# Kernel tuning notes

Hardware: AMD Instinct MI355X
Metric: run time of the kernel (lower is better)

Reference implementation:

```python
import jax, jax.numpy as jnp
import numpy as np

N = 100000   # number of nodes
E = 400000   # number of edges
C = 16       # n_in_channels == n_out_channels
L = 16       # node_conv2 .. node_conv17
EPS = 1e-5   # BatchNorm eps


def _bn(h, g, b):
    # training-mode BatchNorm1d over the edge/batch axis (biased variance)
    mu = h.mean(0)
    var = h.var(0)
    return (h - mu) * jax.lax.rsqrt(var + EPS) * g + b


def setup_inputs() -> dict:
    key = jax.random.key(0)
    ks = jax.random.split(key, 6)
    return {
        "edge_features": jax.random.normal(ks[0], (E, C), jnp.float32),
        "edge_index": jax.random.randint(ks[1], (2, E), 0, N),
        "angles": jax.random.normal(ks[2], (E,), jnp.float32),
        "Wn": jax.random.normal(ks[3], (L, C, 2 * C), jnp.float32) / np.sqrt(2.0 * C),
        "bn": jnp.zeros((L, C), jnp.float32),
        "gn": jnp.ones((L, C), jnp.float32),
        "btn": jnp.zeros((L, C), jnp.float32),
        "We": jax.random.normal(ks[4], (C, 2 * C), jnp.float32) / np.sqrt(2.0 * C),
        "be": jnp.zeros((C,), jnp.float32),
        "ge": jnp.ones((C,), jnp.float32),
        "bte": jnp.zeros((C,), jnp.float32),
    }


def _forward(edge_features, edge_index, Wn, bn, gn, btn, We, be, ge, bte):
    src, dst = edge_index[0], edge_index[1]

    # EdgeConvNoNodes: init node features = mean of incident edge features (both endpoints)
    idx = jnp.concatenate([src, dst])                       # [2E]
    feats = jnp.concatenate([edge_features, edge_features], axis=0)
    deg = jax.ops.segment_sum(jnp.ones((2 * E,), edge_features.dtype), idx, N)
    x = jax.ops.segment_sum(feats, idx, N) / jnp.clip(deg, 1.0)[:, None]  # [N, C]

    # in-degree for mean aggregation of the 16 NodeConv1 layers
    deg_in = jnp.clip(jax.ops.segment_sum(jnp.ones((E,), x.dtype), dst, N), 1.0)[:, None]

    def step(x, p):
        W, b, g, bt = p
        # message: Linear(cat(x_i, x_j)) -> BN -> LeakyReLU on [E, C]
        m = jnp.concatenate([x[dst], x[src]], axis=1) @ W.T + b
        m = jax.nn.leaky_relu(_bn(m, g, bt))
        # mean aggregation at target nodes
        return jax.ops.segment_sum(m, dst, N) / deg_in, None

    x, _ = jax.lax.scan(step, x, (Wn, bn, gn, btn))

    # EdgeConv2: per-edge MLP on both edge directions, BN stats shared over [2E]
    pair = jnp.concatenate(
        [jnp.concatenate([x[src], x[dst]], axis=1),
         jnp.concatenate([x[dst], x[src]], axis=1)], axis=0)  # [2E, 2C]
    e = jax.nn.leaky_relu(_bn(pair @ We.T + be, ge, bte))      # [2E, C]
    e_fwd, e_bwd = e[:E], e[E:]
    edge_out = 0.5 * (e_fwd + e_bwd)                           # symmetric edge feature
    side_loss = jnp.mean((e_fwd - e_bwd) ** 2)                 # symmetry side loss
    return edge_out, side_loss


def reference(edge_features, edge_index, angles, Wn, bn, gn, btn, We, be, ge, bte):
    # `angles` is accepted but unused, matching the original forward
    return _forward(edge_features, edge_index, Wn, bn, gn, btn, We, be, ge, bte)
```

## Files before the change

### kernel.cpp

```cpp
#include <hip/hip_runtime.h>
#include <hip/hip_fp16.h>
#include <cstdint>
#include <cstddef>

#define NN 100000
#define EE 400000
#define CC 16
#define LL 16
#define NB 8

typedef unsigned int uint;

__device__ __forceinline__ float lrelu(float v){ return v > 0.0f ? v : 0.01f*v; }

__device__ __forceinline__ float waveSum(float v){
#pragma unroll
  for (int off = 32; off >= 1; off >>= 1) v += __shfl_xor(v, off);
  return v;
}

__device__ __forceinline__ float fma4(float4 w, float4 v, float a){
  a = fmaf(w.x, v.x, a); a = fmaf(w.y, v.y, a);
  a = fmaf(w.z, v.z, a); a = fmaf(w.w, v.w, a);
  return a;
}

__device__ __forceinline__ uint pack_h2(float a, float b){
  __half2 h = __floats2half2_rn(a, b);
  return *reinterpret_cast<uint*>(&h);
}
__device__ __forceinline__ float2 unpack_h2(uint v){
  __half2 h = *reinterpret_cast<__half2*>(&v);
  return __half22float2(h);
}

__global__ __launch_bounds__(256) void k_count(const int* __restrict__ ei,
    int* __restrict__ cdst, int* __restrict__ call)
{
  int t = blockIdx.x*256 + threadIdx.x;
  if (t >= EE) return;
  int s = ei[t], d = ei[EE + t];
  atomicAdd(&cdst[d], 1);
  atomicAdd(&call[s], 1);
  atomicAdd(&call[d], 1);
}

__device__ __forceinline__ void scan_one(const int* __restrict__ cnt,
    int* __restrict__ rp, int* __restrict__ bsums, int n, int* sd)
{
  int tid = threadIdx.x;
  int base = blockIdx.x*1024 + tid*4;
  int v0=0,v1=0,v2=0,v3=0;
  if (base+0 < n) v0 = cnt[base+0];
  if (base+1 < n) v1 = cnt[base+1];
  if (base+2 < n) v2 = cnt[base+2];
  if (base+3 < n) v3 = cnt[base+3];
  int tot = v0+v1+v2+v3;
  sd[tid] = tot; __syncthreads();
  for (int off=1; off<256; off<<=1){
    int add = (tid>=off) ? sd[tid-off] : 0;
    __syncthreads();
    sd[tid] += add;
    __syncthreads();
  }
  int excl = sd[tid] - tot;
  if (base+0 < n) rp[base+0] = excl;
  if (base+1 < n) rp[base+1] = excl+v0;
  if (base+2 < n) rp[base+2] = excl+v0+v1;
  if (base+3 < n) rp[base+3] = excl+v0+v1+v2;
  if (tid==255) bsums[blockIdx.x] = sd[255];
  __syncthreads();
}

__global__ __launch_bounds__(256) void k_scan1(const int* __restrict__ ca,
    int* __restrict__ rpa, int* __restrict__ bsa,
    const int* __restrict__ cb, int* __restrict__ rpb, int* __restrict__ bsb, int n)
{
  __shared__ int sd[256];
  scan_one(ca, rpa, bsa, n, sd);
  scan_one(cb, rpb, bsb, n, sd);
}

__device__ __forceinline__ void scan2_one(const int* __restrict__ bsums,
    int* __restrict__ boff, int nseg, int* sd)
{
  int tid = threadIdx.x;
  int v = (tid < nseg) ? bsums[tid] : 0;
  sd[tid] = v; __syncthreads();
  for (int off=1; off<256; off<<=1){
    int add = (tid>=off) ? sd[tid-off] : 0;
    __syncthreads();
    sd[tid] += add;
    __syncthreads();
  }
  if (tid < nseg) boff[tid] = sd[tid] - v;
  __syncthreads();
}

__global__ __launch_bounds__(256) void k_scan2(const int* __restrict__ bsa,
    int* __restrict__ boffa, const int* __restrict__ bsb, int* __restrict__ boffb, int nseg)
{
  __shared__ int sd[256];
  scan2_one(bsa, boffa, nseg, sd);
  scan2_one(bsb, boffb, nseg, sd);
}

__global__ __launch_bounds__(256) void k_scan3(
    int* __restrict__ rpa, int* __restrict__ cura, const int* __restrict__ boffa, int totala,
    int* __restrict__ rpb, int* __restrict__ curb, const int* __restrict__ boffb, int totalb, int n)
{
  int adda = boffa[blockIdx.x];
  int addb = boffb[blockIdx.x];
  int base = blockIdx.x*1024 + threadIdx.x*4;
#pragma unroll
  for (int i=0;i<4;i++){
    if (base+i < n){
      int va = rpa[base+i] + adda; rpa[base+i] = va; cura[base+i] = va;
      int vb = rpb[base+i] + addb; rpb[base+i] = vb; curb[base+i] = vb;
    }
  }
  if (blockIdx.x==0 && threadIdx.x==0){ rpa[n] = totala; rpb[n] = totalb; }
}

__global__ __launch_bounds__(256) void k_fill(const int* __restrict__ ei,
    int* __restrict__ cur, int2* __restrict__ sd,
    int* __restrict__ cur_all, int* __restrict__ list_all)
{
  int t = blockIdx.x*256 + threadIdx.x;
  if (t >= EE) return;
  int s = ei[t], d = ei[EE + t];
  int p = atomicAdd(&cur[d], 1);
  sd[p] = make_int2(s, d);
  int pa = atomicAdd(&cur_all[s], 1);
  list_all[pa] = t;
  int pb = atomicAdd(&cur_all[d], 1);
  list_all[pb] = t;
}

__global__ __launch_bounds__(256) void k_gather0(const float* __restrict__ ef,
    const int* __restrict__ rp_all, const int* __restrict__ list_all,
    const int* __restrict__ rp, float* __restrict__ x0, float* __restrict__ invdeg)
{
  int t = blockIdx.x*256 + threadIdx.x;
  if (t >= NN*CC) return;
  int n = t >> 4, c = t & 15;
  int beg = rp_all[n], end = rp_all[n+1];
  float acc = 0.0f;
  for (int i=beg; i<end; i++){
    acc += ef[(size_t)list_all[i]*CC + c];
  }
  float dg = fmaxf((float)(end-beg), 1.0f);
  x0[t] = acc / dg;
  if (c == 0){
    int di = rp[n+1] - rp[n];
    invdeg[n] = 1.0f / fmaxf((float)di, 1.0f);
  }
}

__global__ __launch_bounds__(256) void k_edge(const float* __restrict__ x,
    const int2* __restrict__ sd,
    const float* __restrict__ W, const float* __restrict__ b,
    uint* __restrict__ mh, double* __restrict__ st)
{
  __shared__ float sW[512];
  __shared__ float sb16[16];
  __shared__ float sredS[64], sredQ[64];
  for (int i=threadIdx.x; i<512; i+=256) sW[i] = W[i];
  if (threadIdx.x < 16) sb16[threadIdx.x] = b[threadIdx.x];
  __syncthreads();

  int t = blockIdx.x*256 + threadIdx.x;
  int e0 = 2*t, e1 = 2*t+1;
  bool val = (e1 < EE);
  float acc0[16], acc1[16];
  if (val){
    int2 p0 = sd[e0], p1 = sd[e1];
    float4 xc0[8], xc1[8];
    const float4* p;
    p = (const float4*)(x + (size_t)p0.y*CC); xc0[0]=p[0]; xc0[1]=p[1]; xc0[2]=p[2]; xc0[3]=p[3];
    p = (const float4*)(x + (size_t)p0.x*CC); xc0[4]=p[0]; xc0[5]=p[1]; xc0[6]=p[2]; xc0[7]=p[3];
    p = (const float4*)(x + (size_t)p1.y*CC); xc1[0]=p[0]; xc1[1]=p[1]; xc1[2]=p[2]; xc1[3]=p[3];
    p = (const float4*)(x + (size_t)p1.x*CC); xc1[4]=p[0]; xc1[5]=p[1]; xc1[6]=p[2]; xc1[7]=p[3];
#pragma unroll
    for (int c=0;c<CC;c++){
      const float4* wr = (const float4*)(sW + c*32);
      float a0 = sb16[c], a1 = sb16[c];
#pragma unroll
      for (int q=0;q<8;q++){
        float4 w = wr[q];
        a0 = fma4(w, xc0[q], a0);
        a1 = fma4(w, xc1[q], a1);
      }
      acc0[c]=a0; acc1[c]=a1;
    }
    uint w0[8], w1[8];
#pragma unroll
    for (int q=0;q<8;q++){
      w0[q] = pack_h2(acc0[2*q], acc0[2*q+1]);
      w1[q] = pack_h2(acc1[2*q], acc1[2*q+1]);
    }
    uint4* po0 = (uint4*)(mh + (size_t)e0*8);
    po0[0] = make_uint4(w0[0],w0[1],w0[2],w0[3]);
    po0[1] = make_uint4(w0[4],w0[5],w0[6],w0[7]);
    uint4* po1 = (uint4*)(mh + (size_t)e1*8);
    po1[0] = make_uint4(w1[0],w1[1],w1[2],w1[3]);
    po1[1] = make_uint4(w1[4],w1[5],w1[6],w1[7]);
  } else {
#pragma unroll
    for (int c=0;c<CC;c++){ acc0[c]=0.0f; acc1[c]=0.0f; }
  }

  int lane = threadIdx.x & 63, w = threadIdx.x >> 6;
#pragma unroll
  for (int c=0;c<CC;c++){
    float rs = acc0[c] + acc1[c];
    float rq = acc0[c]*acc0[c] + acc1[c]*acc1[c];
    rs = waveSum(rs); rq = waveSum(rq);
    if (lane == 0){ sredS[w*16+c] = rs; sredQ[w*16+c] = rq; }
  }
  __syncthreads();
  double* stb = st + (size_t)(blockIdx.x & (NB-1))*32;
  if (threadIdx.x < 16){
    int c = threadIdx.x;
    float tot = sredS[c] + sredS[16+c] + sredS[32+c] + sredS[48+c];
    unsafeAtomicAdd(&stb[c], (double)tot);
  } else if (threadIdx.x < 32){
    int c = threadIdx.x - 16;
    float tot = sredQ[c] + sredQ[16+c] + sredQ[32+c] + sredQ[48+c];
    unsafeAtomicAdd(&stb[16+c], (double)tot);
  }
}

__global__ __launch_bounds__(256) void k_node(const uint* __restrict__ mh,
    const int* __restrict__ rp,
    const float* __restrict__ invdeg, const double* __restrict__ st,
    const float* __restrict__ g, const float* __restrict__ bt,
    float* __restrict__ xout)
{
  __shared__ float sA[16], sB[16];
  if (threadIdx.x < 16){
    int c = threadIdx.x;
    double S = 0.0, Q = 0.0;
#pragma unroll
    for (int k=0;k<NB;k++){ S += st[k*32 + c]; Q += st[k*32 + 16 + c]; }
    double mu  = S * (1.0/EE);
    double var = Q * (1.0/EE) - mu*mu;
    float sc = rsqrtf((float)var + 1e-5f);
    float A = sc * g[c];
    sA[c] = A; sB[c] = bt[c] - (float)mu * A;
  }
  __syncthreads();
  int t = blockIdx.x*256 + threadIdx.x;
  int n = t >> 3, cp = t & 7;
  if (n >= NN) return;
  float A0 = sA[2*cp], B0 = sB[2*cp];
  float A1 = sA[2*cp+1], B1 = sB[2*cp+1];
  int beg = rp[n], end = rp[n+1];
  float a0 = 0.0f, a1 = 0.0f;
  for (int i=beg; i<end; i++){
    float2 v = unpack_h2(mh[(size_t)i*8 + cp]);
    a0 += lrelu(fmaf(A0, v.x, B0));
    a1 += lrelu(fmaf(A1, v.y, B1));
  }
  float iv = invdeg[n];
  float2* po = (float2*)(xout + (size_t)n*CC + 2*cp);
  *po = make_float2(a0*iv, a1*iv);
}

__global__ __launch_bounds__(256) void k_final1(const float* __restrict__ x,
    const int* __restrict__ ei, const float* __restrict__ W, const float* __restrict__ b,
    double* __restrict__ st)
{
  __shared__ float sW[512];
  __shared__ float sb16[16];
  __shared__ float sredS[64], sredQ[64];
  for (int i=threadIdx.x; i<512; i+=256) sW[i] = W[i];
  if (threadIdx.x < 16) sb16[threadIdx.x] = b[threadIdx.x];
  __syncthreads();

  int t = blockIdx.x*256 + threadIdx.x;
  bool val = (t < EE);
  float af[16], ab[16];
  if (val){
    int s = ei[t], d = ei[EE+t];
    float4 xs[4], xd[4];
    const float4* p;
    p = (const float4*)(x + (size_t)s*CC); xs[0]=p[0]; xs[1]=p[1]; xs[2]=p[2]; xs[3]=p[3];
    p = (const float4*)(x + (size_t)d*CC); xd[0]=p[0]; xd[1]=p[1]; xd[2]=p[2]; xd[3]=p[3];
#pragma unroll
    for (int c=0;c<CC;c++){
      const float4* wr = (const float4*)(sW + c*32);
      float f = sb16[c], g_ = sb16[c];
#pragma unroll
      for (int q=0;q<4;q++){ float4 w = wr[q];   f = fma4(w, xs[q], f);  g_ = fma4(w, xd[q], g_); }
#pragma unroll
      for (int q=0;q<4;q++){ float4 w = wr[4+q]; f = fma4(w, xd[q], f);  g_ = fma4(w, xs[q], g_); }
      af[c]=f; ab[c]=g_;
    }
  } else {
#pragma unroll
    for (int c=0;c<CC;c++){ af[c]=0.0f; ab[c]=0.0f; }
  }

  int lane = threadIdx.x & 63, w = threadIdx.x >> 6;
#pragma unroll
  for (int c=0;c<CC;c++){
    float rs = af[c] + ab[c];
    float rq = af[c]*af[c] + ab[c]*ab[c];
    rs = waveSum(rs); rq = waveSum(rq);
    if (lane == 0){ sredS[w*16+c] = rs; sredQ[w*16+c] = rq; }
  }
  __syncthreads();
  double* stb = st + (size_t)(blockIdx.x & (NB-1))*32;
  if (threadIdx.x < 16){
    int c = threadIdx.x;
    float tot = sredS[c] + sredS[16+c] + sredS[32+c] + sredS[48+c];
    unsafeAtomicAdd(&stb[c], (double)tot);
  } else if (threadIdx.x < 32){
    int c = threadIdx.x - 16;
    float tot = sredQ[c] + sredQ[16+c] + sredQ[32+c] + sredQ[48+c];
    unsafeAtomicAdd(&stb[16+c], (double)tot);
  }
}

__global__ __launch_bounds__(256) void k_final2(const float* __restrict__ x,
    const int* __restrict__ ei, const float* __restrict__ W, const float* __restrict__ b,
    const double* __restrict__ st, const float* __restrict__ g, const float* __restrict__ bt,
    float* __restrict__ out, double* __restrict__ loss)
{
  __shared__ float sW[512];
  __shared__ float sb16[16];
  __shared__ float sA[16], sB[16];
  __shared__ float sl[4];
  for (int i=threadIdx.x; i<512; i+=256) sW[i] = W[i];
  if (threadIdx.x < 16){
    int c = threadIdx.x;
    sb16[c] = b[c];
    double S = 0.0, Q = 0.0;
#pragma unroll
    for (int k=0;k<NB;k++){ S += st[k*32 + c]; Q += st[k*32 + 16 + c]; }
    double mu  = S * (1.0/(2.0*EE));
    double var = Q * (1.0/(2.0*EE)) - mu*mu;
    float sc = rsqrtf((float)var + 1e-5f);
    float A = sc * g[c];
    sA[c] = A; sB[c] = bt[c] - (float)mu * A;
  }
  __syncthreads();

  int t = blockIdx.x*256 + threadIdx.x;
  bool val = (t < EE);
  float lsum = 0.0f;
  if (val){
    int s = ei[t], d = ei[EE+t];
    float4 xs[4], xd[4];
    const float4* p;
    p = (const float4*)(x + (size_t)s*CC); xs[0]=p[0]; xs[1]=p[1]; xs[2]=p[2]; xs[3]=p[3];
    p = (const float4*)(x + (size_t)d*CC); xd[0]=p[0]; xd[1]=p[1]; xd[2]=p[2]; xd[3]=p[3];
    float fo[16];
#pragma unroll
    for (int c=0;c<CC;c++){
      const float4* wr = (const float4*)(sW + c*32);
      float f = sb16[c], g_ = sb16[c];
#pragma unroll
      for (int q=0;q<4;q++){ float4 w = wr[q];   f = fma4(w, xs[q], f);  g_ = fma4(w, xd[q], g_); }
#pragma unroll
      for (int q=0;q<4;q++){ float4 w = wr[4+q]; f = fma4(w, xd[q], f);  g_ = fma4(w, xs[q], g_); }
      float efv = lrelu(fmaf(sA[c], f,  sB[c]));
      float ebv = lrelu(fmaf(sA[c], g_, sB[c]));
      fo[c] = 0.5f*(efv + ebv);
      float dlt = efv - ebv;
      lsum = fmaf(dlt, dlt, lsum);
    }
    float4* po = (float4*)(out + (size_t)t*CC);
    po[0]=make_float4(fo[0],fo[1],fo[2],fo[3]);
    po[1]=make_float4(fo[4],fo[5],fo[6],fo[7]);
    po[2]=make_float4(fo[8],fo[9],fo[10],fo[11]);
    po[3]=make_float4(fo[12],fo[13],fo[14],fo[15]);
  }
  lsum = waveSum(lsum);
  int lane = threadIdx.x & 63, w = threadIdx.x >> 6;
  if (lane == 0) sl[w] = lsum;
  __syncthreads();
  if (threadIdx.x == 0)
    unsafeAtomicAdd(&loss[blockIdx.x & (NB-1)], (double)(sl[0]+sl[1]+sl[2]+sl[3]));
}

__global__ void k_final3(float* __restrict__ out, const double* __restrict__ loss)
{
  double s = 0.0;
#pragma unroll
  for (int k=0;k<NB;k++) s += loss[k];
  out[(size_t)EE*CC] = (float)(s * (1.0/((double)EE*CC)));
}

extern "C" void kernel_launch(void* const* d_in, const int* in_sizes, int n_in,
                              void* d_out, int out_size, void* d_ws, size_t ws_size,
                              hipStream_t stream)
{
  (void)in_sizes; (void)n_in; (void)out_size; (void)ws_size;
  const float* ef  = (const float*)d_in[0];
  const int*   ei  = (const int*)d_in[1];
  const float* Wn  = (const float*)d_in[3];
  const float* bn  = (const float*)d_in[4];
  const float* gn  = (const float*)d_in[5];
  const float* btn = (const float*)d_in[6];
  const float* We  = (const float*)d_in[7];
  const float* be  = (const float*)d_in[8];
  const float* ge  = (const float*)d_in[9];
  const float* bte = (const float*)d_in[10];
  float* out = (float*)d_out;
  char* ws = (char*)d_ws;

  size_t off = 0;
  auto alloc = [&](size_t bytes)->size_t{
    size_t r = off; off = (off + bytes + 255) & ~(size_t)255; return r;
  };
  size_t o_xa     = alloc((size_t)NN*CC*4);
  size_t o_xb     = alloc((size_t)NN*CC*4);
  size_t o_mh     = alloc((size_t)EE*8*4);
  size_t o_cdst   = alloc((size_t)NN*4);
  size_t o_call   = alloc((size_t)NN*4);
  size_t o_rp     = alloc((size_t)(NN+1)*4);
  size_t o_rpall  = alloc((size_t)(NN+1)*4);
  size_t o_cur    = alloc((size_t)NN*4);
  size_t o_curall = alloc((size_t)NN*4);
  size_t o_sd     = alloc((size_t)EE*8);
  size_t o_listall= alloc((size_t)2*EE*4);
  size_t o_bsum   = alloc(512);
  size_t o_bsum2  = alloc(512);
  size_t o_boff   = alloc(512);
  size_t o_boff2  = alloc(512);
  size_t o_stats  = alloc((size_t)(17*NB*32 + NB)*8);
  size_t o_invdeg = alloc((size_t)NN*4);

  float*  x_a     = (float*)(ws + o_xa);
  float*  x_b     = (float*)(ws + o_xb);
  uint*   m_h     = (uint*)(ws + o_mh);
  int*    cdst    = (int*)(ws + o_cdst);
  int*    call_   = (int*)(ws + o_call);
  int*    rp      = (int*)(ws + o_rp);
  int*    rp_all  = (int*)(ws + o_rpall);
  int*    cur     = (int*)(ws + o_cur);
  int*    cur_all = (int*)(ws + o_curall);
  int2*   sd      = (int2*)(ws + o_sd);
  int*    list_all= (int*)(ws + o_listall);
  int*    bsum    = (int*)(ws + o_bsum);
  int*    bsum2   = (int*)(ws + o_bsum2);
  int*    boff    = (int*)(ws + o_boff);
  int*    boff2   = (int*)(ws + o_boff2);
  double* stats   = (double*)(ws + o_stats);
  double* lossd   = stats + (size_t)17*NB*32;
  float*  invdeg  = (float*)(ws + o_invdeg);

  const int GB_E  = (EE + 255)/256;
  const int GB_E2 = (EE/2 + 255)/256;
  const int GB_NC = (NN*CC + 255)/256;
  const int GB_N8 = (NN*8 + 255)/256;
  const int NSEG  = (NN + 1023)/1024;

  hipMemsetAsync(cdst, 0, (size_t)NN*4, stream);
  hipMemsetAsync(call_, 0, (size_t)NN*4, stream);
  hipMemsetAsync(stats, 0, (size_t)(17*NB*32 + NB)*8, stream);

  k_count<<<GB_E, 256, 0, stream>>>(ei, cdst, call_);
  k_scan1<<<NSEG, 256, 0, stream>>>(cdst, rp, bsum, call_, rp_all, bsum2, NN);
  k_scan2<<<1, 256, 0, stream>>>(bsum, boff, bsum2, boff2, NSEG);
  k_scan3<<<NSEG, 256, 0, stream>>>(rp, cur, boff, EE, rp_all, cur_all, boff2, 2*EE, NN);
  k_fill<<<GB_E, 256, 0, stream>>>(ei, cur, sd, cur_all, list_all);
  k_gather0<<<GB_NC, 256, 0, stream>>>(ef, rp_all, list_all, rp, x_a, invdeg);

  const float* xc = x_a;
  float* xn = x_b;
  for (int l = 0; l < LL; ++l){
    double* st = stats + (size_t)l*NB*32;
    const float* Wl = Wn + (size_t)l*CC*2*CC;
    const float* bl = bn + (size_t)l*CC;
    k_edge<<<GB_E2, 256, 0, stream>>>(xc, sd, Wl, bl, m_h, st);
    k_node<<<GB_N8, 256, 0, stream>>>(m_h, rp, invdeg, st,
                                      gn + (size_t)l*CC, btn + (size_t)l*CC, xn);
    float* tmp = (float*)xc; xc = xn; xn = tmp;
  }

  double* stF = stats + (size_t)16*NB*32;
  k_final1<<<GB_E, 256, 0, stream>>>(xc, ei, We, be, stF);
  k_final2<<<GB_E, 256, 0, stream>>>(xc, ei, We, be, stF, ge, bte, out, lossd);
  k_final3<<<1, 1, 0, stream>>>(out, lossd);
}
```

Before: 865.4 us.

## Fuse all layers and final edge MLP into one cooperative persistent kernel

Replaces the 34 per-layer edge/node/final kernel launches with a single cooperative kernel that loops over layers, using grid.sync between the BN-statistics and aggregation phases. Each block owns a contiguous node range and its incoming edges, so messages are kept in LDS (up to 1024 edges per block) rather than going through global memory, spilling to global only on overflow. It adds grid-wide barriers and limits parallelism to one resident grid (at most 1024 blocks), and falls back to the old multi-kernel path if the cooperative launch fails.

```diff
diff --git a/kernel.cpp b/kernel.cpp
--- a/kernel.cpp
+++ b/kernel.cpp
@@ -1,5 +1,6 @@
 #include <hip/hip_runtime.h>
 #include <hip/hip_fp16.h>
+#include <hip/hip_cooperative_groups.h>
 #include <cstdint>
 #include <cstddef>
 
@@ -8,7 +9,10 @@
 #define CC 16
 #define LL 16
 #define NB 8
-
+#define CAP 1024
+#define CSTR 1032
+
+namespace cg = cooperative_groups;
 typedef unsigned int uint;
 
 __device__ __forceinline__ float lrelu(float v){ return v > 0.0f ? v : 0.01f*v; }
@@ -157,7 +161,246 @@
   }
 }
 
-__global__ __launch_bounds__(256) void k_edge(const float* __restrict__ x,
+__global__ __launch_bounds__(256) void k_layers(
+    float* __restrict__ xa, float* __restrict__ xb,
+    const int2* __restrict__ sd, const int* __restrict__ rp,
+    const float* __restrict__ invdeg, const int* __restrict__ ei,
+    const float* __restrict__ Wn, const float* __restrict__ bn,
+    const float* __restrict__ gn, const float* __restrict__ btn,
+    const float* __restrict__ We, const float* __restrict__ be,
+    const float* __restrict__ ge, const float* __restrict__ bte,
+    double* __restrict__ stats, double* __restrict__ lossd,
+    uint* __restrict__ mspill, float* __restrict__ out)
+{
+  cg::grid_group grid = cg::this_grid();
+  __shared__ float sW[512];
+  __shared__ float sb[16];
+  __shared__ float sAB[32];
+  __shared__ float sredS[64], sredQ[64];
+  __shared__ float sl[4];
+  __shared__ uint  sM[8*CSTR];
+
+  const int tid = threadIdx.x;
+  const int bid = blockIdx.x;
+  const int nblk = gridDim.x;
+  const int npb = (NN + nblk - 1) / nblk;
+  int nlo = bid * npb; if (nlo > NN) nlo = NN;
+  int nhi = nlo + npb; if (nhi > NN) nhi = NN;
+  const int ebeg = rp[nlo];
+  const int eend = rp[nhi];
+
+  const float* xc = xa;
+  float* xn = xb;
+
+  float ls[16], lq[16];
+
+  for (int l = 0; l < LL; ++l){
+    const float* W = Wn + (size_t)l*512;
+    for (int i = tid; i < 512; i += 256) sW[i] = W[i];
+    if (tid < 16) sb[tid] = bn[l*16 + tid];
+    __syncthreads();
+
+#pragma unroll
+    for (int c=0;c<16;c++){ ls[c]=0.f; lq[c]=0.f; }
+
+    for (int i = ebeg + tid; i < eend; i += 256){
+      int2 p = sd[i];
+      const float4* xd4 = (const float4*)(xc + (size_t)p.y*CC);
+      const float4* xs4 = (const float4*)(xc + (size_t)p.x*CC);
+      float4 xd0=xd4[0], xd1=xd4[1], xd2=xd4[2], xd3=xd4[3];
+      float4 xs0=xs4[0], xs1=xs4[1], xs2=xs4[2], xs3=xs4[3];
+      int slot = i - ebeg;
+      bool inl = slot < CAP;
+      uint* gsp = mspill + (size_t)i*8;
+#pragma unroll
+      for (int q = 0; q < 8; ++q){
+        const int c = 2*q;
+        const float4* w0 = (const float4*)(sW + c*32);
+        const float4* w1 = (const float4*)(sW + c*32 + 32);
+        float a0 = sb[c], a1 = sb[c+1];
+        a0 = fma4(w0[0],xd0,a0); a0 = fma4(w0[1],xd1,a0);
+        a0 = fma4(w0[2],xd2,a0); a0 = fma4(w0[3],xd3,a0);
+        a0 = fma4(w0[4],xs0,a0); a0 = fma4(w0[5],xs1,a0);
+        a0 = fma4(w0[6],xs2,a0); a0 = fma4(w0[7],xs3,a0);
+        a1 = fma4(w1[0],xd0,a1); a1 = fma4(w1[1],xd1,a1);
+        a1 = fma4(w1[2],xd2,a1); a1 = fma4(w1[3],xd3,a1);
+        a1 = fma4(w1[4],xs0,a1); a1 = fma4(w1[5],xs1,a1);
+        a1 = fma4(w1[6],xs2,a1); a1 = fma4(w1[7],xs3,a1);
+        ls[c]   += a0; lq[c]   += a0*a0;
+        ls[c+1] += a1; lq[c+1] += a1*a1;
+        uint pk = pack_h2(a0, a1);
+        if (inl) sM[q*CSTR + slot] = pk; else gsp[q] = pk;
+      }
+    }
+
+    {
+      int lane = tid & 63, w = tid >> 6;
+#pragma unroll
+      for (int c=0;c<16;c++){
+        float rs = waveSum(ls[c]);
+        float rq = waveSum(lq[c]);
+        if (lane==0){ sredS[w*16+c]=rs; sredQ[w*16+c]=rq; }
+      }
+      __syncthreads();
+      double* stb = stats + (size_t)l*NB*32 + (size_t)(bid & (NB-1))*32;
+      if (tid < 16){
+        float tot = sredS[tid]+sredS[16+tid]+sredS[32+tid]+sredS[48+tid];
+        unsafeAtomicAdd(&stb[tid], (double)tot);
+      } else if (tid < 32){
+        int c = tid-16;
+        float tot = sredQ[c]+sredQ[16+c]+sredQ[32+c]+sredQ[48+c];
+        unsafeAtomicAdd(&stb[16+c], (double)tot);
+      }
+    }
+    __threadfence();
+    grid.sync();
+
+    if (tid < 16){
+      const double* stl = stats + (size_t)l*NB*32;
+      double S=0.0, Q=0.0;
+#pragma unroll
+      for (int k=0;k<NB;k++){ S += stl[k*32+tid]; Q += stl[k*32+16+tid]; }
+      double mu  = S * (1.0/EE);
+      double var = Q * (1.0/EE) - mu*mu;
+      float sc = rsqrtf((float)var + 1e-5f);
+      float A = sc * gn[l*16+tid];
+      sAB[tid] = A; sAB[16+tid] = btn[l*16+tid] - (float)mu * A;
+    }
+    __syncthreads();
+
+    for (int u = tid; u < npb*8; u += 256){
+      int n = nlo + (u>>3);
+      if (n >= nhi) break;
+      int cp = u & 7;
+      float A0=sAB[2*cp],   B0=sAB[16+2*cp];
+      float A1=sAB[2*cp+1], B1=sAB[16+2*cp+1];
+      int beg = rp[n], end = rp[n+1];
+      float a0=0.f, a1=0.f;
+      for (int i=beg; i<end; ++i){
+        int slot = i - ebeg;
+        uint v = (slot < CAP) ? sM[cp*CSTR + slot] : mspill[(size_t)i*8 + cp];
+        float2 f = unpack_h2(v);
+        a0 += lrelu(fmaf(A0, f.x, B0));
+        a1 += lrelu(fmaf(A1, f.y, B1));
+      }
+      float iv = invdeg[n];
+      *(float2*)(xn + (size_t)n*CC + 2*cp) = make_float2(a0*iv, a1*iv);
+    }
+    __threadfence();
+    grid.sync();
+    const float* t = xc; xc = xn; xn = (float*)t;
+  }
+
+  for (int i = tid; i < 512; i += 256) sW[i] = We[i];
+  if (tid < 16) sb[tid] = be[tid];
+  __syncthreads();
+
+  const int epb = (EE + nblk - 1) / nblk;
+  int fb = bid*epb; if (fb > EE) fb = EE;
+  int fe = fb + epb; if (fe > EE) fe = EE;
+
+#pragma unroll
+  for (int c=0;c<16;c++){ ls[c]=0.f; lq[c]=0.f; }
+  for (int t_ = fb + tid; t_ < fe; t_ += 256){
+    int s = ei[t_], d = ei[EE+t_];
+    const float4* ps = (const float4*)(xc + (size_t)s*CC);
+    const float4* pd = (const float4*)(xc + (size_t)d*CC);
+    float4 xs0=ps[0], xs1=ps[1], xs2=ps[2], xs3=ps[3];
+    float4 xd0=pd[0], xd1=pd[1], xd2=pd[2], xd3=pd[3];
+#pragma unroll
+    for (int c=0;c<16;c++){
+      const float4* wr = (const float4*)(sW + c*32);
+      float f = sb[c], g_ = sb[c];
+      f  = fma4(wr[0],xs0,f);  f  = fma4(wr[1],xs1,f);
+      f  = fma4(wr[2],xs2,f);  f  = fma4(wr[3],xs3,f);
+      f  = fma4(wr[4],xd0,f);  f  = fma4(wr[5],xd1,f);
+      f  = fma4(wr[6],xd2,f);  f  = fma4(wr[7],xd3,f);
+      g_ = fma4(wr[0],xd0,g_); g_ = fma4(wr[1],xd1,g_);
+      g_ = fma4(wr[2],xd2,g_); g_ = fma4(wr[3],xd3,g_);
+      g_ = fma4(wr[4],xs0,g_); g_ = fma4(wr[5],xs1,g_);
+      g_ = fma4(wr[6],xs2,g_); g_ = fma4(wr[7],xs3,g_);
+      ls[c] += f + g_;
+      lq[c] += f*f + g_*g_;
+    }
+  }
+  {
+    int lane = tid & 63, w = tid >> 6;
+#pragma unroll
+    for (int c=0;c<16;c++){
+      float rs = waveSum(ls[c]);
+      float rq = waveSum(lq[c]);
+      if (lane==0){ sredS[w*16+c]=rs; sredQ[w*16+c]=rq; }
+    }
+    __syncthreads();
+    double* stb = stats + (size_t)LL*NB*32 + (size_t)(bid & (NB-1))*32;
+    if (tid < 16){
+      float tot = sredS[tid]+sredS[16+tid]+sredS[32+tid]+sredS[48+tid];
+      unsafeAtomicAdd(&stb[tid], (double)tot);
+    } else if (tid < 32){
+      int c = tid-16;
+      float tot = sredQ[c]+sredQ[16+c]+sredQ[32+c]+sredQ[48+c];
+      unsafeAtomicAdd(&stb[16+c], (double)tot);
+    }
+  }
+  __threadfence();
+  grid.sync();
+
+  if (tid < 16){
+    const double* stl = stats + (size_t)LL*NB*32;
+    double S=0.0, Q=0.0;
+#pragma unroll
+    for (int k=0;k<NB;k++){ S += stl[k*32+tid]; Q += stl[k*32+16+tid]; }
+    double mu  = S * (1.0/(2.0*EE));
+    double var = Q * (1.0/(2.0*EE)) - mu*mu;
+    float sc = rsqrtf((float)var + 1e-5f);
+    float A = sc * ge[tid];
+    sAB[tid] = A; sAB[16+tid] = bte[tid] - (float)mu * A;
+  }
+  __syncthreads();
+
+  float lsum = 0.0f;
+  for (int t_ = fb + tid; t_ < fe; t_ += 256){
+    int s = ei[t_], d = ei[EE+t_];
+    const float4* ps = (const float4*)(xc + (size_t)s*CC);
+    const float4* pd = (const float4*)(xc + (size_t)d*CC);
+    float4 xs0=ps[0], xs1=ps[1], xs2=ps[2], xs3=ps[3];
+    float4 xd0=pd[0], xd1=pd[1], xd2=pd[2], xd3=pd[3];
+    float fo[16];
+#pragma unroll
+    for (int c=0;c<16;c++){
+      const float4* wr = (const float4*)(sW + c*32);
+      float f = sb[c], g_ = sb[c];
+      f  = fma4(wr[0],xs0,f);  f  = fma4(wr[1],xs1,f);
+      f  = fma4(wr[2],xs2,f);  f  = fma4(wr[3],xs3,f);
+      f  = fma4(wr[4],xd0,f);  f  = fma4(wr[5],xd1,f);
+      f  = fma4(wr[6],xd2,f);  f  = fma4(wr[7],xd3,f);
+      g_ = fma4(wr[0],xd0,g_); g_ = fma4(wr[1],xd1,g_);
+      g_ = fma4(wr[2],xd2,g_); g_ = fma4(wr[3],xd3,g_);
+      g_ = fma4(wr[4],xs0,g_); g_ = fma4(wr[5],xs1,g_);
+      g_ = fma4(wr[6],xs2,g_); g_ = fma4(wr[7],xs3,g_);
+      float efv = lrelu(fmaf(sAB[c], f,  sAB[16+c]));
+      float ebv = lrelu(fmaf(sAB[c], g_, sAB[16+c]));
+      fo[c] = 0.5f*(efv + ebv);
+      float dlt = efv - ebv;
+      lsum = fmaf(dlt, dlt, lsum);
+    }
+    float4* po = (float4*)(out + (size_t)t_*CC);
+    po[0]=make_float4(fo[0],fo[1],fo[2],fo[3]);
+    po[1]=make_float4(fo[4],fo[5],fo[6],fo[7]);
+    po[2]=make_float4(fo[8],fo[9],fo[10],fo[11]);
+    po[3]=make_float4(fo[12],fo[13],fo[14],fo[15]);
+  }
+  lsum = waveSum(lsum);
+  {
+    int lane = tid & 63, w = tid >> 6;
+    if (lane == 0) sl[w] = lsum;
+    __syncthreads();
+    if (tid == 0)
+      unsafeAtomicAdd(&lossd[bid & (NB-1)], (double)(sl[0]+sl[1]+sl[2]+sl[3]));
+  }
+}
+
+__global__ __launch_bounds__(256) void k_edge_fb(const float* __restrict__ x,
     const int2* __restrict__ sd,
     const float* __restrict__ W, const float* __restrict__ b,
     uint* __restrict__ mh, double* __restrict__ st)
@@ -231,7 +474,7 @@
   }
 }
 
-__global__ __launch_bounds__(256) void k_node(const uint* __restrict__ mh,
+__global__ __launch_bounds__(256) void k_node_fb(const uint* __restrict__ mh,
     const int* __restrict__ rp,
     const float* __restrict__ invdeg, const double* __restrict__ st,
     const float* __restrict__ g, const float* __restrict__ bt,
@@ -267,7 +510,7 @@
   *po = make_float2(a0*iv, a1*iv);
 }
 
-__global__ __launch_bounds__(256) void k_final1(const float* __restrict__ x,
+__global__ __launch_bounds__(256) void k_final1_fb(const float* __restrict__ x,
     const int* __restrict__ ei, const float* __restrict__ W, const float* __restrict__ b,
     double* __restrict__ st)
 {
@@ -323,7 +566,7 @@
   }
 }
 
-__global__ __launch_bounds__(256) void k_final2(const float* __restrict__ x,
+__global__ __launch_bounds__(256) void k_final2_fb(const float* __restrict__ x,
     const int* __restrict__ ei, const float* __restrict__ W, const float* __restrict__ b,
     const double* __restrict__ st, const float* __restrict__ g, const float* __restrict__ bt,
     float* __restrict__ out, double* __restrict__ loss)
@@ -469,20 +712,40 @@
   k_fill<<<GB_E, 256, 0, stream>>>(ei, cur, sd, cur_all, list_all);
   k_gather0<<<GB_NC, 256, 0, stream>>>(ef, rp_all, list_all, rp, x_a, invdeg);
 
-  const float* xc = x_a;
-  float* xn = x_b;
-  for (int l = 0; l < LL; ++l){
-    double* st = stats + (size_t)l*NB*32;
-    const float* Wl = Wn + (size_t)l*CC*2*CC;
-    const float* bl = bn + (size_t)l*CC;
-    k_edge<<<GB_E2, 256, 0, stream>>>(xc, sd, Wl, bl, m_h, st);
-    k_node<<<GB_N8, 256, 0, stream>>>(m_h, rp, invdeg, st,
-                                      gn + (size_t)l*CC, btn + (size_t)l*CC, xn);
-    float* tmp = (float*)xc; xc = xn; xn = tmp;
-  }
-
-  double* stF = stats + (size_t)16*NB*32;
-  k_final1<<<GB_E, 256, 0, stream>>>(xc, ei, We, be, stF);
-  k_final2<<<GB_E, 256, 0, stream>>>(xc, ei, We, be, stF, ge, bte, out, lossd);
+  int occ = 0, cus = 0, dev = 0;
+  (void)hipGetDevice(&dev);
+  (void)hipDeviceGetAttribute(&cus, hipDeviceAttributeMultiprocessorCount, dev);
+  (void)hipOccupancyMaxActiveBlocksPerMultiprocessor(&occ, (const void*)k_layers, 256, 0);
+  long maxg = (long)occ * (long)(cus > 0 ? cus : 0);
+  int grid = (int)(maxg > 1024 ? 1024 : maxg);
+
+  hipError_t cerr = hipErrorUnknown;
+  if (grid >= 64){
+    void* args[] = {
+      (void*)&x_a, (void*)&x_b, (void*)&sd, (void*)&rp, (void*)&invdeg, (void*)&ei,
+      (void*)&Wn, (void*)&bn, (void*)&gn, (void*)&btn,
+      (void*)&We, (void*)&be, (void*)&ge, (void*)&bte,
+      (void*)&stats, (void*)&lossd, (void*)&m_h, (void*)&out
+    };
+    cerr = hipLaunchCooperativeKernel((void*)k_layers, dim3(grid), dim3(256), args, 0, stream);
+  }
+
+  if (cerr != hipSuccess){
+    const float* xc = x_a;
+    float* xn = x_b;
+    for (int l = 0; l < LL; ++l){
+      double* st = stats + (size_t)l*NB*32;
+      const float* Wl = Wn + (size_t)l*CC*2*CC;
+      const float* bl = bn + (size_t)l*CC;
+      k_edge_fb<<<GB_E2, 256, 0, stream>>>(xc, sd, Wl, bl, m_h, st);
+      k_node_fb<<<GB_N8, 256, 0, stream>>>(m_h, rp, invdeg, st,
+                                           gn + (size_t)l*CC, btn + (size_t)l*CC, xn);
+      float* tmp = (float*)xc; xc = xn; xn = tmp;
+    }
+    double* stF = stats + (size_t)LL*NB*32;
+    k_final1_fb<<<GB_E, 256, 0, stream>>>(xc, ei, We, be, stF);
+    k_final2_fb<<<GB_E, 256, 0, stream>>>(xc, ei, We, be, stF, ge, bte, out, lossd);
+  }
+
   k_final3<<<1, 1, 0, stream>>>(out, lossd);
 }
```

Result: no change. 867.5 us (+0.2%).

## Split edge linear into per-node U/V projections and fuse next-layer projection into aggregation

Applied to the files above, without the earlier changes.

Because W·cat(x_dst, x_src) = W1·x_dst + W2·x_src, the per-edge 16x32 matvec becomes two per-node projections (u, v), stored in fp16 and summed per edge. The per-edge message buffer disappears. A stats kernel gathers u[dst] and v[src] to accumulate the BatchNorm sums, and the node kernel recomputes each message from u and v during aggregation. The node kernel also computes the next layer's u and v from the new x through shared memory, so the per-layer matmul cost drops from E to N rows. In exchange every edge is gathered twice per layer, and the pre-BN message is now rounded from the sum of two fp16 values.

```diff
diff --git a/kernel.cpp b/kernel.cpp
--- a/kernel.cpp
+++ b/kernel.cpp
@@ -157,65 +157,77 @@
   }
 }
 
-__global__ __launch_bounds__(256) void k_edge(const float* __restrict__ x,
-    const int2* __restrict__ sd,
+__global__ __launch_bounds__(256) void k_uv(const float* __restrict__ x,
     const float* __restrict__ W, const float* __restrict__ b,
-    uint* __restrict__ mh, double* __restrict__ st)
+    uint* __restrict__ u, uint* __restrict__ v)
 {
   __shared__ float sW[512];
   __shared__ float sb16[16];
-  __shared__ float sredS[64], sredQ[64];
   for (int i=threadIdx.x; i<512; i+=256) sW[i] = W[i];
   if (threadIdx.x < 16) sb16[threadIdx.x] = b[threadIdx.x];
   __syncthreads();
-
+  int n = blockIdx.x*256 + threadIdx.x;
+  if (n >= NN) return;
+  const float4* xr = (const float4*)(x + (size_t)n*CC);
+  float4 x0 = xr[0], x1 = xr[1], x2 = xr[2], x3 = xr[3];
+  uint up[8], vp[8];
+#pragma unroll
+  for (int q=0;q<8;q++){
+    int c0 = 2*q, c1 = 2*q+1;
+    const float4* w0 = (const float4*)(sW + c0*32);
+    const float4* w1 = (const float4*)(sW + c1*32);
+    float u0 = sb16[c0], u1 = sb16[c1], v0 = 0.f, v1 = 0.f;
+    u0 = fma4(w0[0],x0,u0); u0 = fma4(w0[1],x1,u0); u0 = fma4(w0[2],x2,u0); u0 = fma4(w0[3],x3,u0);
+    v0 = fma4(w0[4],x0,v0); v0 = fma4(w0[5],x1,v0); v0 = fma4(w0[6],x2,v0); v0 = fma4(w0[7],x3,v0);
+    u1 = fma4(w1[0],x0,u1); u1 = fma4(w1[1],x1,u1); u1 = fma4(w1[2],x2,u1); u1 = fma4(w1[3],x3,u1);
+    v1 = fma4(w1[4],x0,v1); v1 = fma4(w1[5],x1,v1); v1 = fma4(w1[6],x2,v1); v1 = fma4(w1[7],x3,v1);
+    up[q] = pack_h2(u0,u1);
+    vp[q] = pack_h2(v0,v1);
+  }
+  uint4* pu = (uint4*)(u + (size_t)n*8);
+  pu[0] = make_uint4(up[0],up[1],up[2],up[3]);
+  pu[1] = make_uint4(up[4],up[5],up[6],up[7]);
+  uint4* pv = (uint4*)(v + (size_t)n*8);
+  pv[0] = make_uint4(vp[0],vp[1],vp[2],vp[3]);
+  pv[1] = make_uint4(vp[4],vp[5],vp[6],vp[7]);
+}
+
+__global__ __launch_bounds__(256) void k_stat(
+    const uint* __restrict__ u, const uint* __restrict__ v,
+    const int2* __restrict__ sd, double* __restrict__ st)
+{
+  __shared__ float sredS[64], sredQ[64];
   int t = blockIdx.x*256 + threadIdx.x;
-  int e0 = 2*t, e1 = 2*t+1;
-  bool val = (e1 < EE);
-  float acc0[16], acc1[16];
-  if (val){
-    int2 p0 = sd[e0], p1 = sd[e1];
-    float4 xc0[8], xc1[8];
-    const float4* p;
-    p = (const float4*)(x + (size_t)p0.y*CC); xc0[0]=p[0]; xc0[1]=p[1]; xc0[2]=p[2]; xc0[3]=p[3];
-    p = (const float4*)(x + (size_t)p0.x*CC); xc0[4]=p[0]; xc0[5]=p[1]; xc0[6]=p[2]; xc0[7]=p[3];
-    p = (const float4*)(x + (size_t)p1.y*CC); xc1[0]=p[0]; xc1[1]=p[1]; xc1[2]=p[2]; xc1[3]=p[3];
-    p = (const float4*)(x + (size_t)p1.x*CC); xc1[4]=p[0]; xc1[5]=p[1]; xc1[6]=p[2]; xc1[7]=p[3];
-#pragma unroll
-    for (int c=0;c<CC;c++){
-      const float4* wr = (const float4*)(sW + c*32);
-      float a0 = sb16[c], a1 = sb16[c];
+  float ls[16], lq[16];
+#pragma unroll
+  for (int c=0;c<16;c++){ ls[c]=0.f; lq[c]=0.f; }
+#pragma unroll
+  for (int k=0;k<2;k++){
+    int e = 2*t + k;
+    if (e < EE){
+      int2 p = sd[e];
+      const uint4* pu = (const uint4*)(u + (size_t)p.y*8);
+      const uint4* pv = (const uint4*)(v + (size_t)p.x*8);
+      uint4 ua = pu[0], ub = pu[1];
+      uint4 va = pv[0], vb = pv[1];
+      uint uw[8] = {ua.x,ua.y,ua.z,ua.w, ub.x,ub.y,ub.z,ub.w};
+      uint vw[8] = {va.x,va.y,va.z,va.w, vb.x,vb.y,vb.z,vb.w};
 #pragma unroll
       for (int q=0;q<8;q++){
-        float4 w = wr[q];
-        a0 = fma4(w, xc0[q], a0);
-        a1 = fma4(w, xc1[q], a1);
+        float2 fu = unpack_h2(uw[q]);
+        float2 fv = unpack_h2(vw[q]);
+        float m0 = fu.x + fv.x;
+        float m1 = fu.y + fv.y;
+        ls[2*q]   += m0; lq[2*q]   += m0*m0;
+        ls[2*q+1] += m1; lq[2*q+1] += m1*m1;
       }
-      acc0[c]=a0; acc1[c]=a1;
     }
-    uint w0[8], w1[8];
-#pragma unroll
-    for (int q=0;q<8;q++){
-      w0[q] = pack_h2(acc0[2*q], acc0[2*q+1]);
-      w1[q] = pack_h2(acc1[2*q], acc1[2*q+1]);
-    }
-    uint4* po0 = (uint4*)(mh + (size_t)e0*8);
-    po0[0] = make_uint4(w0[0],w0[1],w0[2],w0[3]);
-    po0[1] = make_uint4(w0[4],w0[5],w0[6],w0[7]);
-    uint4* po1 = (uint4*)(mh + (size_t)e1*8);
-    po1[0] = make_uint4(w1[0],w1[1],w1[2],w1[3]);
-    po1[1] = make_uint4(w1[4],w1[5],w1[6],w1[7]);
-  } else {
-#pragma unroll
-    for (int c=0;c<CC;c++){ acc0[c]=0.0f; acc1[c]=0.0f; }
-  }
-
+  }
   int lane = threadIdx.x & 63, w = threadIdx.x >> 6;
 #pragma unroll
-  for (int c=0;c<CC;c++){
-    float rs = acc0[c] + acc1[c];
-    float rq = acc0[c]*acc0[c] + acc1[c]*acc1[c];
-    rs = waveSum(rs); rq = waveSum(rq);
+  for (int c=0;c<16;c++){
+    float rs = waveSum(ls[c]);
+    float rq = waveSum(lq[c]);
     if (lane == 0){ sredS[w*16+c] = rs; sredQ[w*16+c] = rq; }
   }
   __syncthreads();
@@ -231,15 +243,26 @@
   }
 }
 
-__global__ __launch_bounds__(256) void k_node(const uint* __restrict__ mh,
-    const int* __restrict__ rp,
+template<bool LAST>
+__global__ __launch_bounds__(256) void k_node_uv(
+    const uint* __restrict__ u, const uint* __restrict__ v,
+    const int2* __restrict__ sd, const int* __restrict__ rp,
     const float* __restrict__ invdeg, const double* __restrict__ st,
     const float* __restrict__ g, const float* __restrict__ bt,
-    float* __restrict__ xout)
+    const float* __restrict__ Wnx, const float* __restrict__ bnx,
+    uint* __restrict__ unx, uint* __restrict__ vnx, float* __restrict__ xout)
 {
   __shared__ float sA[16], sB[16];
-  if (threadIdx.x < 16){
-    int c = threadIdx.x;
+  __shared__ float sW[512];
+  __shared__ float sbn[16];
+  __shared__ float sX[32][17];
+  const int tid = threadIdx.x;
+  if (!LAST){
+    for (int i=tid;i<512;i+=256) sW[i] = Wnx[i];
+    if (tid < 16) sbn[tid] = bnx[tid];
+  }
+  if (tid < 16){
+    int c = tid;
     double S = 0.0, Q = 0.0;
 #pragma unroll
     for (int k=0;k<NB;k++){ S += st[k*32 + c]; Q += st[k*32 + 16 + c]; }
@@ -250,21 +273,44 @@
     sA[c] = A; sB[c] = bt[c] - (float)mu * A;
   }
   __syncthreads();
-  int t = blockIdx.x*256 + threadIdx.x;
-  int n = t >> 3, cp = t & 7;
-  if (n >= NN) return;
-  float A0 = sA[2*cp], B0 = sB[2*cp];
+
+  int t = blockIdx.x*256 + tid;
+  int n = t >> 3, cp = t & 7, nl = tid >> 3;
+  float A0 = sA[2*cp],   B0 = sB[2*cp];
   float A1 = sA[2*cp+1], B1 = sB[2*cp+1];
+  float2 uu = unpack_h2(u[(size_t)n*8 + cp]);
   int beg = rp[n], end = rp[n+1];
-  float a0 = 0.0f, a1 = 0.0f;
-  for (int i=beg; i<end; i++){
-    float2 v = unpack_h2(mh[(size_t)i*8 + cp]);
-    a0 += lrelu(fmaf(A0, v.x, B0));
-    a1 += lrelu(fmaf(A1, v.y, B1));
+  float a0 = 0.f, a1 = 0.f;
+  for (int i=beg; i<end; ++i){
+    int s = sd[i].x;
+    float2 fv = unpack_h2(v[(size_t)s*8 + cp]);
+    a0 += lrelu(fmaf(A0, uu.x + fv.x, B0));
+    a1 += lrelu(fmaf(A1, uu.y + fv.y, B1));
   }
   float iv = invdeg[n];
-  float2* po = (float2*)(xout + (size_t)n*CC + 2*cp);
-  *po = make_float2(a0*iv, a1*iv);
+  float xv0 = a0*iv, xv1 = a1*iv;
+
+  if (LAST){
+    *(float2*)(xout + (size_t)n*CC + 2*cp) = make_float2(xv0, xv1);
+  } else {
+    sX[nl][2*cp] = xv0; sX[nl][2*cp+1] = xv1;
+    __syncthreads();
+    int c0 = 2*cp, c1 = 2*cp+1;
+    const float* w0 = sW + c0*32;
+    const float* w1 = sW + c1*32;
+    const float* xr = sX[nl];
+    float un0 = sbn[c0], un1 = sbn[c1], vn0 = 0.f, vn1 = 0.f;
+#pragma unroll
+    for (int k=0;k<16;k++){
+      float xv = xr[k];
+      un0 = fmaf(w0[k],    xv, un0);
+      vn0 = fmaf(w0[16+k], xv, vn0);
+      un1 = fmaf(w1[k],    xv, un1);
+      vn1 = fmaf(w1[16+k], xv, vn1);
+    }
+    unx[(size_t)n*8 + cp] = pack_h2(un0, un1);
+    vnx[(size_t)n*8 + cp] = pack_h2(vn0, vn1);
+  }
 }
 
 __global__ __launch_bounds__(256) void k_final1(const float* __restrict__ x,
@@ -416,8 +462,10 @@
     size_t r = off; off = (off + bytes + 255) & ~(size_t)255; return r;
   };
   size_t o_xa     = alloc((size_t)NN*CC*4);
-  size_t o_xb     = alloc((size_t)NN*CC*4);
-  size_t o_mh     = alloc((size_t)EE*8*4);
+  size_t o_ua     = alloc((size_t)NN*8*4);
+  size_t o_va     = alloc((size_t)NN*8*4);
+  size_t o_ub     = alloc((size_t)NN*8*4);
+  size_t o_vb     = alloc((size_t)NN*8*4);
   size_t o_cdst   = alloc((size_t)NN*4);
   size_t o_call   = alloc((size_t)NN*4);
   size_t o_rp     = alloc((size_t)(NN+1)*4);
@@ -434,8 +482,10 @@
   size_t o_invdeg = alloc((size_t)NN*4);
 
   float*  x_a     = (float*)(ws + o_xa);
-  float*  x_b     = (float*)(ws + o_xb);
-  uint*   m_h     = (uint*)(ws + o_mh);
+  uint*   u_a     = (uint*)(ws + o_ua);
+  uint*   v_a     = (uint*)(ws + o_va);
+  uint*   u_b     = (uint*)(ws + o_ub);
+  uint*   v_b     = (uint*)(ws + o_vb);
   int*    cdst    = (int*)(ws + o_cdst);
   int*    call_   = (int*)(ws + o_call);
   int*    rp      = (int*)(ws + o_rp);
@@ -455,7 +505,8 @@
   const int GB_E  = (EE + 255)/256;
   const int GB_E2 = (EE/2 + 255)/256;
   const int GB_NC = (NN*CC + 255)/256;
-  const int GB_N8 = (NN*8 + 255)/256;
+  const int GB_N8 = (NN*8)/256;
+  const int GB_N  = (NN + 255)/256;
   const int NSEG  = (NN + 1023)/1024;
 
   hipMemsetAsync(cdst, 0, (size_t)NN*4, stream);
@@ -468,21 +519,29 @@
   k_scan3<<<NSEG, 256, 0, stream>>>(rp, cur, boff, EE, rp_all, cur_all, boff2, 2*EE, NN);
   k_fill<<<GB_E, 256, 0, stream>>>(ei, cur, sd, cur_all, list_all);
   k_gather0<<<GB_NC, 256, 0, stream>>>(ef, rp_all, list_all, rp, x_a, invdeg);
-
-  const float* xc = x_a;
-  float* xn = x_b;
+  k_uv<<<GB_N, 256, 0, stream>>>(x_a, Wn, bn, u_a, v_a);
+
+  uint* uc = u_a; uint* vc = v_a;
+  uint* un = u_b; uint* vn = v_b;
   for (int l = 0; l < LL; ++l){
     double* st = stats + (size_t)l*NB*32;
-    const float* Wl = Wn + (size_t)l*CC*2*CC;
-    const float* bl = bn + (size_t)l*CC;
-    k_edge<<<GB_E2, 256, 0, stream>>>(xc, sd, Wl, bl, m_h, st);
-    k_node<<<GB_N8, 256, 0, stream>>>(m_h, rp, invdeg, st,
-                                      gn + (size_t)l*CC, btn + (size_t)l*CC, xn);
-    float* tmp = (float*)xc; xc = xn; xn = tmp;
-  }
-
-  double* stF = stats + (size_t)16*NB*32;
-  k_final1<<<GB_E, 256, 0, stream>>>(xc, ei, We, be, stF);
-  k_final2<<<GB_E, 256, 0, stream>>>(xc, ei, We, be, stF, ge, bte, out, lossd);
+    k_stat<<<GB_E2, 256, 0, stream>>>(uc, vc, sd, st);
+    if (l < LL-1){
+      k_node_uv<false><<<GB_N8, 256, 0, stream>>>(uc, vc, sd, rp, invdeg, st,
+          gn + (size_t)l*CC, btn + (size_t)l*CC,
+          Wn + (size_t)(l+1)*CC*2*CC, bn + (size_t)(l+1)*CC,
+          un, vn, nullptr);
+      uint* t1 = uc; uc = un; un = t1;
+      uint* t2 = vc; vc = vn; vn = t2;
+    } else {
+      k_node_uv<true><<<GB_N8, 256, 0, stream>>>(uc, vc, sd, rp, invdeg, st,
+          gn + (size_t)l*CC, btn + (size_t)l*CC,
+          nullptr, nullptr, nullptr, nullptr, x_a);
+    }
+  }
+
+  double* stF = stats + (size_t)LL*NB*32;
+  k_final1<<<GB_E, 256, 0, stream>>>(x_a, ei, We, be, stF);
+  k_final2<<<GB_E, 256, 0, stream>>>(x_a, ei, We, be, stF, ge, bte, out, lossd);
   k_final3<<<1, 1, 0, stream>>>(out, lossd);
 }
```

Result: slower. 960.8 us (+11.0%).

## Partition edge kernel by destination-node blocks and widen stats atomic spread

Applied to the files above, without the earlier changes.

The per-layer edge kernel now assigns each block a range of 32 destination nodes and loops over their CSR edge range, one edge per thread with strided iteration, instead of two edges per thread over a flat grid. Both edge and node kernels launch NN/32 blocks, and the BN statistics atomics are spread across 32 slots instead of 8 to reduce contention. The goal is fewer double-atomic collisions and more uniform per-thread work. The cost is load imbalance from varying per-block edge counts. The node kernel's bounds check is dropped because the grid now divides NN exactly.

```diff
diff --git a/kernel.cpp b/kernel.cpp
--- a/kernel.cpp
+++ b/kernel.cpp
@@ -7,7 +7,8 @@
 #define EE 400000
 #define CC 16
 #define LL 16
-#define NB 8
+#define NB 32
+#define NPB 32
 
 typedef unsigned int uint;
 
@@ -158,7 +159,7 @@
 }
 
 __global__ __launch_bounds__(256) void k_edge(const float* __restrict__ x,
-    const int2* __restrict__ sd,
+    const int2* __restrict__ sd, const int* __restrict__ rp,
     const float* __restrict__ W, const float* __restrict__ b,
     uint* __restrict__ mh, double* __restrict__ st)
 {
@@ -169,53 +170,48 @@
   if (threadIdx.x < 16) sb16[threadIdx.x] = b[threadIdx.x];
   __syncthreads();
 
-  int t = blockIdx.x*256 + threadIdx.x;
-  int e0 = 2*t, e1 = 2*t+1;
-  bool val = (e1 < EE);
-  float acc0[16], acc1[16];
-  if (val){
-    int2 p0 = sd[e0], p1 = sd[e1];
-    float4 xc0[8], xc1[8];
-    const float4* p;
-    p = (const float4*)(x + (size_t)p0.y*CC); xc0[0]=p[0]; xc0[1]=p[1]; xc0[2]=p[2]; xc0[3]=p[3];
-    p = (const float4*)(x + (size_t)p0.x*CC); xc0[4]=p[0]; xc0[5]=p[1]; xc0[6]=p[2]; xc0[7]=p[3];
-    p = (const float4*)(x + (size_t)p1.y*CC); xc1[0]=p[0]; xc1[1]=p[1]; xc1[2]=p[2]; xc1[3]=p[3];
-    p = (const float4*)(x + (size_t)p1.x*CC); xc1[4]=p[0]; xc1[5]=p[1]; xc1[6]=p[2]; xc1[7]=p[3];
-#pragma unroll
-    for (int c=0;c<CC;c++){
-      const float4* wr = (const float4*)(sW + c*32);
-      float a0 = sb16[c], a1 = sb16[c];
-#pragma unroll
-      for (int q=0;q<8;q++){
-        float4 w = wr[q];
-        a0 = fma4(w, xc0[q], a0);
-        a1 = fma4(w, xc1[q], a1);
-      }
-      acc0[c]=a0; acc1[c]=a1;
+  int nlo = blockIdx.x * NPB;
+  int elo = rp[nlo], ehi = rp[nlo + NPB];
+
+  float ls[16], lq[16];
+#pragma unroll
+  for (int c=0;c<16;c++){ ls[c]=0.f; lq[c]=0.f; }
+
+  for (int i = elo + threadIdx.x; i < ehi; i += 256){
+    int2 p = sd[i];
+    const float4* xd4 = (const float4*)(x + (size_t)p.y*CC);
+    const float4* xs4 = (const float4*)(x + (size_t)p.x*CC);
+    float4 xd0=xd4[0], xd1=xd4[1], xd2=xd4[2], xd3=xd4[3];
+    float4 xs0=xs4[0], xs1=xs4[1], xs2=xs4[2], xs3=xs4[3];
+    uint pk[8];
+#pragma unroll
+    for (int q=0;q<8;q++){
+      int c0 = 2*q, c1 = 2*q+1;
+      const float4* w0 = (const float4*)(sW + c0*32);
+      const float4* w1 = (const float4*)(sW + c1*32);
+      float a0 = sb16[c0], a1 = sb16[c1];
+      a0 = fma4(w0[0],xd0,a0); a0 = fma4(w0[1],xd1,a0);
+      a0 = fma4(w0[2],xd2,a0); a0 = fma4(w0[3],xd3,a0);
+      a0 = fma4(w0[4],xs0,a0); a0 = fma4(w0[5],xs1,a0);
+      a0 = fma4(w0[6],xs2,a0); a0 = fma4(w0[7],xs3,a0);
+      a1 = fma4(w1[0],xd0,a1); a1 = fma4(w1[1],xd1,a1);
+      a1 = fma4(w1[2],xd2,a1); a1 = fma4(w1[3],xd3,a1);
+      a1 = fma4(w1[4],xs0,a1); a1 = fma4(w1[5],xs1,a1);
+      a1 = fma4(w1[6],xs2,a1); a1 = fma4(w1[7],xs3,a1);
+      ls[c0] += a0; lq[c0] += a0*a0;
+      ls[c1] += a1; lq[c1] += a1*a1;
+      pk[q] = pack_h2(a0, a1);
     }
-    uint w0[8], w1[8];
-#pragma unroll
-    for (int q=0;q<8;q++){
-      w0[q] = pack_h2(acc0[2*q], acc0[2*q+1]);
-      w1[q] = pack_h2(acc1[2*q], acc1[2*q+1]);
-    }
-    uint4* po0 = (uint4*)(mh + (size_t)e0*8);
-    po0[0] = make_uint4(w0[0],w0[1],w0[2],w0[3]);
-    po0[1] = make_uint4(w0[4],w0[5],w0[6],w0[7]);
-    uint4* po1 = (uint4*)(mh + (size_t)e1*8);
-    po1[0] = make_uint4(w1[0],w1[1],w1[2],w1[3]);
-    po1[1] = make_uint4(w1[4],w1[5],w1[6],w1[7]);
-  } else {
-#pragma unroll
-    for (int c=0;c<CC;c++){ acc0[c]=0.0f; acc1[c]=0.0f; }
+    uint4* po = (uint4*)(mh + (size_t)i*8);
+    po[0] = make_uint4(pk[0],pk[1],pk[2],pk[3]);
+    po[1] = make_uint4(pk[4],pk[5],pk[6],pk[7]);
   }
 
   int lane = threadIdx.x & 63, w = threadIdx.x >> 6;
 #pragma unroll
-  for (int c=0;c<CC;c++){
-    float rs = acc0[c] + acc1[c];
-    float rq = acc0[c]*acc0[c] + acc1[c]*acc1[c];
-    rs = waveSum(rs); rq = waveSum(rq);
+  for (int c=0;c<16;c++){
+    float rs = waveSum(ls[c]);
+    float rq = waveSum(lq[c]);
     if (lane == 0){ sredS[w*16+c] = rs; sredQ[w*16+c] = rq; }
   }
   __syncthreads();
@@ -252,7 +248,6 @@
   __syncthreads();
   int t = blockIdx.x*256 + threadIdx.x;
   int n = t >> 3, cp = t & 7;
-  if (n >= NN) return;
   float A0 = sA[2*cp], B0 = sB[2*cp];
   float A1 = sA[2*cp+1], B1 = sB[2*cp+1];
   int beg = rp[n], end = rp[n+1];
@@ -453,9 +448,8 @@
   float*  invdeg  = (float*)(ws + o_invdeg);
 
   const int GB_E  = (EE + 255)/256;
-  const int GB_E2 = (EE/2 + 255)/256;
   const int GB_NC = (NN*CC + 255)/256;
-  const int GB_N8 = (NN*8 + 255)/256;
+  const int GB_NB = NN/NPB;
   const int NSEG  = (NN + 1023)/1024;
 
   hipMemsetAsync(cdst, 0, (size_t)NN*4, stream);
@@ -475,13 +469,13 @@
     double* st = stats + (size_t)l*NB*32;
     const float* Wl = Wn + (size_t)l*CC*2*CC;
     const float* bl = bn + (size_t)l*CC;
-    k_edge<<<GB_E2, 256, 0, stream>>>(xc, sd, Wl, bl, m_h, st);
-    k_node<<<GB_N8, 256, 0, stream>>>(m_h, rp, invdeg, st,
+    k_edge<<<GB_NB, 256, 0, stream>>>(xc, sd, rp, Wl, bl, m_h, st);
+    k_node<<<GB_NB, 256, 0, stream>>>(m_h, rp, invdeg, st,
                                       gn + (size_t)l*CC, btn + (size_t)l*CC, xn);
     float* tmp = (float*)xc; xc = xn; xn = tmp;
   }
 
-  double* stF = stats + (size_t)16*NB*32;
+  double* stF = stats + (size_t)LL*NB*32;
   k_final1<<<GB_E, 256, 0, stream>>>(xc, ei, We, be, stF);
   k_final2<<<GB_E, 256, 0, stream>>>(xc, ei, We, be, stF, ge, bte, out, lossd);
   k_final3<<<1, 1, 0, stream>>>(out, lossd);
```

Result: slower. 2.788 ms (+222.1%).
